# Kernel tuning notes

Hardware: AMD Instinct MI355X
Metric: run time of the kernel (lower is better)

## Reference

```python
import jax, jax.numpy as jnp
import numpy as np
from jax import lax

B, T, H, W = 4, 8, 14, 14
DIM, NH = 768, 8
HD = DIM // NH            # 96, head dim (= depthwise conv channels)
G = 1                     # global_embed_num
N = T * H * W + 1 + G     # 1570 tokens: [global, cls, spatial]
HID = 4 * DIM
BIG = 1.0e8


def ln(x, g, b, eps=1e-5):
    m = jnp.mean(x, axis=-1, keepdims=True)
    v = jnp.mean(jnp.square(x - m), axis=-1, keepdims=True)
    return (x - m) * jax.lax.rsqrt(v + eps) * g + b


def setup_inputs() -> dict:
    key = jax.random.key(0)
    ks = jax.random.split(key, 12)
    s = 0.02
    inp = {
        "x": jax.random.normal(ks[0], (B, N, DIM), jnp.float32),
        "t": T, "h": H, "w": W,
        "norm1_g": jnp.ones((DIM,), jnp.float32),
        "norm1_b": jnp.zeros((DIM,), jnp.float32),
        "qkv_w": jax.random.normal(ks[1], (3 * DIM, DIM), jnp.float32) * s,
        "qkv_b": jnp.zeros((3 * DIM,), jnp.float32),
        "conv_q": jax.random.normal(ks[2], (HD, 1, 3, 3, 3), jnp.float32) * 0.05,
        "nq_g": jnp.ones((HD,), jnp.float32), "nq_b": jnp.zeros((HD,), jnp.float32),
        "conv_k": jax.random.normal(ks[3], (HD, 1, 3, 3, 3), jnp.float32) * 0.05,
        "nk_g": jnp.ones((HD,), jnp.float32), "nk_b": jnp.zeros((HD,), jnp.float32),
        "conv_v": jax.random.normal(ks[4], (HD, 1, 3, 3, 3), jnp.float32) * 0.05,
        "nv_g": jnp.ones((HD,), jnp.float32), "nv_b": jnp.zeros((HD,), jnp.float32),
        "proj_w": jax.random.normal(ks[5], (DIM, DIM), jnp.float32) * s,
        "proj_b": jnp.zeros((DIM,), jnp.float32),
        "norm2_g": jnp.ones((DIM,), jnp.float32),
        "norm2_b": jnp.zeros((DIM,), jnp.float32),
        "fc1_w": jax.random.normal(ks[6], (HID, DIM), jnp.float32) * s,
        "fc1_b": jnp.zeros((HID,), jnp.float32),
        "fc2_w": jax.random.normal(ks[7], (DIM, HID), jnp.float32) * s,
        "fc2_b": jnp.zeros((DIM,), jnp.float32),
    }
    return inp


def _pool(tok, cw, g, b):
    # tok: [B, NH, N, HD] -> depthwise conv3d per head on spatial tokens, then LN
    glob, cls, body = tok[:, :, :G], tok[:, :, G:G + 1], tok[:, :, G + 1:]
    z = body.reshape(B * NH, T, H, W, HD).transpose(0, 4, 1, 2, 3)  # [BN, C, T, H, W]
    z = lax.conv_general_dilated(z, cw, window_strides=(1, 1, 1),
                                 padding=[(1, 1)] * 3, feature_group_count=HD,
                                 dimension_numbers=("NCDHW", "OIDHW", "NCDHW"))
    z = z.reshape(B, NH, HD, T * H * W).transpose(0, 1, 3, 2)       # [B, NH, L, HD]
    z = jnp.concatenate([glob, cls, z], axis=2)                     # splice cls then global
    return ln(z, g, b)


def reference(x, t, h, w, norm1_g, norm1_b, qkv_w, qkv_b,
              conv_q, nq_g, nq_b, conv_k, nk_g, nk_b, conv_v, nv_g, nv_b,
              proj_w, proj_b, norm2_g, norm2_b, fc1_w, fc1_b, fc2_w, fc2_b):
    scale = HD ** (-0.5)
    xn = ln(x, norm1_g, norm1_b)
    qkv = (xn @ qkv_w.T + qkv_b).reshape(B, N, 3, NH, HD)
    qkv = qkv.transpose(2, 0, 3, 1, 4)            # [3, B, NH, N, HD]
    q = _pool(qkv[0], conv_q, nq_g, nq_b)
    k = _pool(qkv[1], conv_k, nk_g, nk_b)
    v = _pool(qkv[2], conv_v, nv_g, nv_b)

    attn = jnp.einsum("bhnd,bhmd->bhnm", q, k) * scale
    # additive offset: BIG everywhere except diagonal and the global columns (rows >= G)
    eye = jnp.eye(N, dtype=attn.dtype)
    off2 = eye * BIG
    off2 = off2.at[G:, :G].set(BIG)
    offset = BIG - off2                            # [N, N]
    attn = jax.nn.softmax(attn - offset, axis=-1)

    o = jnp.einsum("bhnm,bhmd->bhnd", attn, v)     # [B, NH, N, HD]
    o = o.transpose(0, 2, 1, 3).reshape(B, N, DIM)
    o = o @ proj_w.T + proj_b

    x = x + o                                      # pool_skip is None -> identity skip
    x2 = ln(x, norm2_g, norm2_b)
    mlp = jax.nn.gelu(x2 @ fc1_w.T + fc1_b, approximate=False) @ fc2_w.T + fc2_b
    return x + mlp
```

## Files before the change

### kernel.cpp

```cpp
#include <hip/hip_runtime.h>
#include <hip/hip_bf16.h>
#include <cmath>

using bf16 = __hip_bfloat16;
using bf16x8_t = __attribute__((ext_vector_type(8))) short;
using f32x4_t  = __attribute__((ext_vector_type(4))) float;

constexpr int kT = 8;
constexpr int kDIM = 768, kNH = 8, kHD = 96;
constexpr int kN = 1570;
constexpr int kB = 4;
constexpr int kM = kB * kN;
constexpr int kBNH = kB * kNH;
constexpr long kPoolRows  = (long)kBNH * kN;
constexpr long kPoolElems = kPoolRows * kHD;

struct SegTab { const void* src[22]; long start[23]; };

__global__ void detect_kernel(const unsigned* __restrict__ probe,
                              unsigned* __restrict__ flag) {
  *flag = (probe[0] == 0x3F803F80u) ? 1u : 0u;
}

__global__ void convert_kernel(SegTab tab, bf16* __restrict__ cin,
                               const unsigned* __restrict__ flag, long chunks) {
  const bool isb = (*flag != 0u);
  const long stride = (long)gridDim.x * blockDim.x;
  for (long c = (long)blockIdx.x * blockDim.x + threadIdx.x; c < chunks; c += stride) {
    const long e8 = c * 8;
    int lo = 0, hi = 22;
    while (hi - lo > 1) { int mid = (lo + hi) >> 1; if (e8 >= tab.start[mid]) lo = mid; else hi = mid; }
    const long e = e8 - tab.start[lo];
    if (isb) {
      *(bf16x8_t*)(cin + e8) = *(const bf16x8_t*)((const unsigned short*)tab.src[lo] + e);
    } else {
      const float* s = (const float*)tab.src[lo] + e;
      float4 a = *(const float4*)s;
      float4 b = *(const float4*)(s + 4);
      bf16 r[8];
      r[0] = (bf16)a.x; r[1] = (bf16)a.y; r[2] = (bf16)a.z; r[3] = (bf16)a.w;
      r[4] = (bf16)b.x; r[5] = (bf16)b.y; r[6] = (bf16)b.z; r[7] = (bf16)b.w;
      *(bf16x8_t*)(cin + e8) = *(bf16x8_t*)r;
    }
  }
}

__device__ __forceinline__ void gload_lds16(const bf16* g, bf16* l) {
  __builtin_amdgcn_global_load_lds(
      (const __attribute__((address_space(1))) unsigned int*)g,
      (__attribute__((address_space(3))) unsigned int*)l, 16, 0, 0);
}

template<int EPI, int DUAL>
__launch_bounds__(512, 1)
__global__ void gemm_bt(const bf16* __restrict__ A, const bf16* __restrict__ Wt,
                        const bf16* __restrict__ bias, const bf16* __restrict__ res,
                        bf16* __restrict__ C, float* __restrict__ Cf,
                        const unsigned* __restrict__ flagp,
                        int M, int K, int Nout, int tiles_n)
{
  __shared__ bf16 shm[73728];
  const int tid  = threadIdx.x;
  const int lane = tid & 63;
  const int wv   = tid >> 6;
  const int wr   = wv & 3, wc = wv >> 2;

  const int nwg = gridDim.x;
  const int tiles_m = nwg / tiles_n;
  const int q8 = nwg >> 3, r8 = nwg & 7;
  const int xcd = blockIdx.x & 7, slot = blockIdx.x >> 3;
  const int base = (xcd < r8) ? xcd * (q8 + 1) : r8 * (q8 + 1) + (xcd - r8) * q8;
  const int lin = base + slot;
  const int paired = (tiles_m & ~1) * tiles_n;
  int tmi, tni;
  if (lin < paired) {
    const int grp = lin / (2 * tiles_n);
    const int rem = lin - grp * 2 * tiles_n;
    tmi = grp * 2 + (rem & 1);
    tni = rem >> 1;
  } else {
    tmi = tiles_m - 1;
    tni = lin - paired;
  }
  const long tile_m = (long)tmi * 256;
  const long tile_n = (long)tni * 128;

  bool isb = true;
  if constexpr (DUAL) isb = (*flagp != 0u);

  f32x4_t zero = {0.f, 0.f, 0.f, 0.f};
  f32x4_t acc[4][4];
#pragma unroll
  for (int i = 0; i < 4; ++i)
#pragma unroll
    for (int j = 0; j < 4; ++j) acc[i][j] = zero;

  const int rb = tid >> 3;
  const int g8 = (((tid & 7) ^ (rb & 7))) * 8;
  const bf16* sA[4];
  const bf16* sB[2];
#pragma unroll
  for (int i = 0; i < 4; ++i) {
    long ar = tile_m + rb + i * 64; if (ar > M - 1) ar = M - 1;
    sA[i] = A + ar * K + g8;
  }
#pragma unroll
  for (int i = 0; i < 2; ++i)
    sB[i] = Wt + (tile_n + rb + i * 64) * K + g8;

  auto stage = [&](int kt, int buf) {
    const long koff = (long)kt << 6;
#pragma unroll
    for (int i = 0; i < 4; ++i)
      gload_lds16(sA[i] + koff, shm + buf * 16384 + i * 4096 + tid * 8);
#pragma unroll
    for (int i = 0; i < 2; ++i)
      gload_lds16(sB[i] + koff, shm + 49152 + buf * 8192 + i * 4096 + tid * 8);
  };

  const int j0 = (((lane >> 4) ^ (lane & 7))) * 8;
  const int j1 = ((((lane >> 4) ^ 4)) ^ (lane & 7)) * 8;
  const int rA0 = wr * 64 + (lane & 15);
  const int rB0 = wc * 64 + (lane & 15);

  const int ksteps = K >> 6;
  stage(0, 0);
  stage(1, 1);
  stage(2, 2);
  asm volatile("s_waitcnt vmcnt(12)" ::: "memory");
  __builtin_amdgcn_s_barrier();

#define KSTEP(BUF, DOPF, PFKT, WAITOP)                                         \
  {                                                                            \
    const bf16* ab = shm + (BUF) * 16384;                                      \
    const bf16* bp = shm + 49152 + (BUF) * 8192;                               \
    bf16x8_t a[4][2], bfr[4][2];                                               \
    _Pragma("unroll")                                                          \
    for (int m = 0; m < 4; ++m) {                                              \
      a[m][0]   = *(const bf16x8_t*)&ab[((rA0 + m * 16) << 6) + j0];           \
      a[m][1]   = *(const bf16x8_t*)&ab[((rA0 + m * 16) << 6) + j1];           \
      bfr[m][0] = *(const bf16x8_t*)&bp[((rB0 + m * 16) << 6) + j0];           \
      bfr[m][1] = *(const bf16x8_t*)&bp[((rB0 + m * 16) << 6) + j1];           \
    }                                                                          \
    asm volatile("s_waitcnt lgkmcnt(0)" ::: "memory");                         \
    __builtin_amdgcn_sched_barrier(0);                                         \
    __builtin_amdgcn_s_barrier();                                              \
    if (DOPF) stage((PFKT), (BUF));                                            \
    __builtin_amdgcn_s_setprio(1);                                             \
    _Pragma("unroll")                                                          \
    for (int m = 0; m < 4; ++m)                                                \
      _Pragma("unroll")                                                        \
      for (int n = 0; n < 4; ++n) {                                            \
        acc[m][n] = __builtin_amdgcn_mfma_f32_16x16x32_bf16(a[m][0], bfr[n][0], acc[m][n], 0, 0, 0); \
        acc[m][n] = __builtin_amdgcn_mfma_f32_16x16x32_bf16(a[m][1], bfr[n][1], acc[m][n], 0, 0, 0); \
      }                                                                        \
    __builtin_amdgcn_s_setprio(0);                                             \
    asm volatile(WAITOP ::: "memory");                                         \
    __builtin_amdgcn_s_barrier();                                              \
  }

  int p = 0;
  for (; p + 5 < ksteps; p += 3) {
    KSTEP(0, true, p + 3, "s_waitcnt vmcnt(12)")
    KSTEP(1, true, p + 4, "s_waitcnt vmcnt(12)")
    KSTEP(2, true, p + 5, "s_waitcnt vmcnt(12)")
  }
  KSTEP(0, false, 0, "s_waitcnt vmcnt(6)")
  KSTEP(1, false, 0, "s_waitcnt vmcnt(0)")
  KSTEP(2, false, 0, "s_waitcnt vmcnt(0)")
#undef KSTEP

  {
    const int cB = wc * 64 + (lane & 15);
    const int rB = wr * 64 + ((lane >> 4) << 2);
#pragma unroll
    for (int n = 0; n < 4; ++n) {
      const int col = cB + n * 16;
      const float bv = (float)bias[tile_n + col];
#pragma unroll
      for (int m = 0; m < 4; ++m)
#pragma unroll
        for (int r = 0; r < 4; ++r)
          shm[(rB + m * 16 + r) * 136 + col] = (bf16)(acc[m][n][r] + bv);
    }
  }
  __syncthreads();
#pragma unroll
  for (int it = 0; it < 8; ++it) {
    const int chunk = tid + it * 512;
    const int row = chunk >> 4;
    const int colc = (chunk & 15) * 8;
    const long grow = tile_m + row;
    if (grow < M) {
      const bf16x8_t v8 = *(const bf16x8_t*)&shm[row * 136 + colc];
      const long gcol = tile_n + colc;
      float f[8];
#pragma unroll
      for (int j = 0; j < 8; ++j) {
        unsigned short u = (unsigned short)v8[j];
        f[j] = __uint_as_float((unsigned)u << 16);
      }
      if constexpr (EPI == 1) {
#pragma unroll
        for (int j = 0; j < 8; ++j) {
          const float v2 = f[j];
          const float zarg = 1.59576912160573f * v2 * (1.f + 0.044715f * v2 * v2);
          f[j] = v2 * __builtin_amdgcn_rcpf(1.f + __expf(-zarg));
        }
      } else if constexpr (EPI == 2) {
        const bf16x8_t rv = *(const bf16x8_t*)&res[grow * Nout + gcol];
#pragma unroll
        for (int j = 0; j < 8; ++j) {
          unsigned short u = (unsigned short)rv[j];
          f[j] += __uint_as_float((unsigned)u << 16);
        }
      }
      if (DUAL && !isb) {
        float4 s0 = {f[0], f[1], f[2], f[3]};
        float4 s1 = {f[4], f[5], f[6], f[7]};
        *(float4*)&Cf[grow * Nout + gcol] = s0;
        *(float4*)&Cf[grow * Nout + gcol + 4] = s1;
      } else {
        bf16 o8[8];
#pragma unroll
        for (int j = 0; j < 8; ++j) o8[j] = (bf16)f[j];
        *(bf16x8_t*)&C[grow * Nout + gcol] = *(bf16x8_t*)o8;
      }
    }
  }
}

__global__ void ln768_kernel(const bf16* __restrict__ x, const bf16* __restrict__ g,
                             const bf16* __restrict__ bta, bf16* __restrict__ y)
{
  const long row = blockIdx.x;
  const int tid = threadIdx.x;
  const bf16* xr = x + row * kDIM;
  float v[3];
  float s = 0.f, ss = 0.f;
#pragma unroll
  for (int i = 0; i < 3; ++i) {
    v[i] = (float)xr[tid + i * 256];
    s += v[i]; ss += v[i] * v[i];
  }
#pragma unroll
  for (int off = 32; off; off >>= 1) {
    s  += __shfl_xor(s, off);
    ss += __shfl_xor(ss, off);
  }
  __shared__ float red[8];
  const int wv = tid >> 6;
  if ((tid & 63) == 0) { red[wv] = s; red[4 + wv] = ss; }
  __syncthreads();
  s  = red[0] + red[1] + red[2] + red[3];
  ss = red[4] + red[5] + red[6] + red[7];
  const float mean = s * (1.f / kDIM);
  const float var  = ss * (1.f / kDIM) - mean * mean;
  const float rstd = rsqrtf(var + 1e-5f);
  bf16* yr = y + row * kDIM;
#pragma unroll
  for (int i = 0; i < 3; ++i) {
    const int c = tid + i * 256;
    yr[c] = (bf16)((v[i] - mean) * rstd * (float)g[c] + (float)bta[c]);
  }
}

__launch_bounds__(256, 4)
__global__ void convpool3_kernel(const bf16* __restrict__ qkv,
                                 const bf16* __restrict__ cwq,
                                 const bf16* __restrict__ cwk,
                                 const bf16* __restrict__ cwv,
                                 bf16* __restrict__ pool)
{
  __shared__ bf16 tile[3 * 256 * 16];
  const int t    = blockIdx.x;
  const int bh   = blockIdx.y;
  const int z    = blockIdx.z;
  const int s    = z / 6, cgrp = z - s * 6;
  const int tid  = threadIdx.x;
  const int b    = bh >> 3, h = bh & 7;

  const bf16* src0 = qkv + (long)(b * kN) * 2304 + s * kDIM + h * kHD + cgrp * 16;

  {
    f32x4_t z4 = {0.f, 0.f, 0.f, 0.f};
    for (int i = tid; i < 3072; i += 256)
      *(f32x4_t*)((char*)tile + (long)i * 16) = z4;
  }
  __syncthreads();

  for (int c = tid; c < 1176; c += 256) {
    const int slice = c / 392;
    const int rem   = c - slice * 392;
    const int p     = rem >> 1;
    const int seg   = rem & 1;
    const int tt    = t + slice - 1;
    if ((unsigned)tt < 8u) {
      const int y = p / 14, x = p - y * 14;
      const int n = 2 + tt * 196 + p;
      const bf16x8_t v = *(const bf16x8_t*)(src0 + (long)n * 2304 + seg * 8);
      *(bf16x8_t*)&tile[slice * 4096 + ((y + 1) * 16 + (x + 1)) * 16 + seg * 8] = v;
    }
  }

  const int dpair = tid & 7;
  const int pg    = tid >> 3;
  const int d0    = cgrp * 16 + dpair * 2;
  const bf16* cw  = (s == 0) ? cwq : (s == 1) ? cwk : cwv;
  float w0[27], w1[27];
#pragma unroll
  for (int i = 0; i < 27; ++i) {
    w0[i] = (float)cw[d0 * 27 + i];
    w1[i] = (float)cw[(d0 + 1) * 27 + i];
  }
  __syncthreads();

  bf16* out0 = pool + (long)s * kPoolElems + (long)bh * kN * kHD;
  for (int p = pg; p < 196; p += 32) {
    const int y = p / 14, x = p - y * 14;
    const char* bp = (const char*)tile + ((y * 16 + x) * 16 + dpair * 2) * 2;
    float a0 = 0.f, a1 = 0.f;
#pragma unroll
    for (int dt = 0; dt < 3; ++dt)
#pragma unroll
      for (int dy = 0; dy < 3; ++dy)
#pragma unroll
        for (int dx = 0; dx < 3; ++dx) {
          const unsigned u = *(const unsigned*)(bp + dt * 8192 + dy * 512 + dx * 32);
          const int i = (dt * 3 + dy) * 3 + dx;
          a0 = fmaf(__uint_as_float(u << 16), w0[i], a0);
          a1 = fmaf(__uint_as_float(u & 0xffff0000u), w1[i], a1);
        }
    const int n = 2 + t * 196 + p;
    bf16 r0 = (bf16)a0, r1 = (bf16)a1;
    unsigned pk = ((unsigned)*(unsigned short*)&r1 << 16) | *(unsigned short*)&r0;
    *(unsigned*)((char*)(out0 + (long)n * kHD + d0)) = pk;
  }
  if (t == 0 && tid < 32) {
    const int tok = tid >> 4, dd = tid & 15;
    out0[(long)tok * kHD + cgrp * 16 + dd] = src0[(long)tok * 2304 + dd];
  }
}

__global__ void ln96_kernel(bf16* __restrict__ pool,
                            const bf16* __restrict__ gq, const bf16* __restrict__ bq,
                            const bf16* __restrict__ gk, const bf16* __restrict__ bk,
                            const bf16* __restrict__ gv, const bf16* __restrict__ bv)
{
  const int z = blockIdx.y;
  bf16* buf = pool + (long)z * kPoolElems;
  const bf16* g  = (z == 0) ? gq : (z == 1) ? gk : gv;
  const bf16* be = (z == 0) ? bq : (z == 1) ? bk : bv;
  const long row = (long)blockIdx.x * 4 + (threadIdx.x >> 6);
  if (row >= kPoolRows) return;
  const int lane = threadIdx.x & 63;
  bf16* p = buf + row * kHD;
  float a0 = 0.f, a1 = 0.f;
  if (lane < 48) {
    a0 = (float)p[lane * 2];
    a1 = (float)p[lane * 2 + 1];
  }
  float sSum = a0 + a1, sSq = a0 * a0 + a1 * a1;
#pragma unroll
  for (int off = 32; off; off >>= 1) {
    sSum += __shfl_xor(sSum, off);
    sSq  += __shfl_xor(sSq, off);
  }
  const float mean = sSum * (1.f / 96);
  const float var  = sSq * (1.f / 96) - mean * mean;
  const float rstd = rsqrtf(var + 1e-5f);
  if (lane < 48) {
    p[lane * 2]     = (bf16)((a0 - mean) * rstd * (float)g[lane * 2]     + (float)be[lane * 2]);
    p[lane * 2 + 1] = (bf16)((a1 - mean) * rstd * (float)g[lane * 2 + 1] + (float)be[lane * 2 + 1]);
  }
}

__global__ void attn_kernel(const bf16* __restrict__ pool, bf16* __restrict__ o)
{
  const long idx = (long)blockIdx.x * 4 + (threadIdx.x >> 6);
  if (idx >= kPoolRows) return;
  const int bh = (int)(idx / kN);
  const int i  = (int)(idx - (long)bh * kN);
  const int lane = threadIdx.x & 63;
  const bf16* qrow  = pool + ((long)bh * kN + i) * kHD;
  const bf16* kbase = pool + kPoolElems + (long)bh * kN * kHD;
  const bf16* vbase = pool + 2 * kPoolElems + (long)bh * kN * kHD;
  float q0 = 0, q1 = 0, ki0 = 0, ki1 = 0, k00 = 0, k01 = 0;
  float vi0 = 0, vi1 = 0, v00 = 0, v01 = 0;
  if (lane < 48) {
    const int c = lane * 2;
    q0  = (float)qrow[c];                  q1  = (float)qrow[c + 1];
    ki0 = (float)kbase[(long)i * kHD + c]; ki1 = (float)kbase[(long)i * kHD + c + 1];
    k00 = (float)kbase[c];                 k01 = (float)kbase[c + 1];
    vi0 = (float)vbase[(long)i * kHD + c]; vi1 = (float)vbase[(long)i * kHD + c + 1];
    v00 = (float)vbase[c];                 v01 = (float)vbase[c + 1];
  }
  float ds = q0 * ki0 + q1 * ki1;
  float dg = q0 * k00 + q1 * k01;
#pragma unroll
  for (int off = 32; off; off >>= 1) {
    ds += __shfl_xor(ds, off);
    dg += __shfl_xor(dg, off);
  }
  float o0, o1;
  if (i == 0) { o0 = v00; o1 = v01; }
  else {
    const float scale = 0.10206207261596575f;
    const float l0 = dg * scale, li = ds * scale;
    const float mx = fmaxf(l0, li);
    const float e0 = __expf(l0 - mx), ei = __expf(li - mx);
    const float inv = 1.f / (e0 + ei);
    o0 = (e0 * v00 + ei * vi0) * inv;
    o1 = (e0 * v01 + ei * vi1) * inv;
  }
  if (lane < 48) {
    const int b = bh >> 3, h = bh & 7;
    bf16* orow = o + ((long)b * kN + i) * kDIM + h * kHD + lane * 2;
    orow[0] = (bf16)o0;
    orow[1] = (bf16)o1;
  }
}

extern "C" void kernel_launch(void* const* d_in, const int* in_sizes, int n_in,
                              void* d_out, int out_size, void* d_ws, size_t ws_size,
                              hipStream_t stream)
{
  const int map[22] = {0,4,5,6,7,8,9,10,11,12,13,14,15,16,17,18,19,20,21,22,23,24};

  char* ws = (char*)d_ws;
  unsigned* flag = (unsigned*)ws;

  size_t off = 256;
  auto take = [&](size_t bytes) {
    size_t r = off;
    off += (bytes + 255) & ~(size_t)255;
    return r;
  };

  SegTab tab;
  long total = 0;
  tab.start[0] = 0;
  for (int j = 0; j < 22; ++j) {
    tab.src[j] = d_in[map[j]];
    total += in_sizes[map[j]];
    tab.start[j + 1] = total;
  }

  bf16* cin = (bf16*)(ws + take((size_t)total * 2));

  bf16* cp[22];
  { long acc = 0;
    for (int j = 0; j < 22; ++j) { cp[j] = cin + acc; acc += in_sizes[map[j]]; } }
  bf16* x_c    = cp[0];
  bf16* n1g_c  = cp[1],  *n1b_c = cp[2];
  bf16* qkvw_c = cp[3],  *qkvb_c = cp[4];
  bf16* cwq_c  = cp[5],  *nqg_c = cp[6],  *nqb_c = cp[7];
  bf16* cwk_c  = cp[8],  *nkg_c = cp[9],  *nkb_c = cp[10];
  bf16* cwv_c  = cp[11], *nvg_c = cp[12], *nvb_c = cp[13];
  bf16* projw_c = cp[14], *projb_c = cp[15];
  bf16* n2g_c  = cp[16], *n2b_c = cp[17];
  bf16* fc1w_c = cp[18], *fc1b_c = cp[19];
  bf16* fc2w_c = cp[20], *fc2b_c = cp[21];

  bf16* qkv  = (bf16*)(ws + take(38584320));
  bf16* xn   = (bf16*)(ws + take(9646080));
  bf16* pool = (bf16*)(ws + take(28938240));
  bf16* x1   = (bf16*)(ws + take(9646080));
  bf16* o   = xn;
  bf16* h1  = qkv;
  bf16* x2n = pool;

  bf16*  out_b = (bf16*)d_out;
  float* out_f = (float*)d_out;

  detect_kernel<<<1, 1, 0, stream>>>((const unsigned*)d_in[4], flag);
  convert_kernel<<<2048, 256, 0, stream>>>(tab, cin, flag, total / 8);

  ln768_kernel<<<kM, 256, 0, stream>>>(x_c, n1g_c, n1b_c, xn);
  gemm_bt<0,0><<<25 * 18, 512, 0, stream>>>(xn, qkvw_c, qkvb_c, nullptr, qkv, nullptr, nullptr, kM, 768, 2304, 18);
  convpool3_kernel<<<dim3(kT, kBNH, 18), 256, 0, stream>>>(qkv, cwq_c, cwk_c, cwv_c, pool);
  ln96_kernel<<<dim3((int)((kPoolRows + 3) / 4), 3), 256, 0, stream>>>(pool, nqg_c, nqb_c, nkg_c, nkb_c, nvg_c, nvb_c);
  attn_kernel<<<(int)((kPoolRows + 3) / 4), 256, 0, stream>>>(pool, o);
  gemm_bt<2,0><<<25 * 6, 512, 0, stream>>>(o, projw_c, projb_c, x_c, x1, nullptr, nullptr, kM, 768, 768, 6);
  ln768_kernel<<<kM, 256, 0, stream>>>(x1, n2g_c, n2b_c, x2n);
  gemm_bt<1,0><<<25 * 24, 512, 0, stream>>>(x2n, fc1w_c, fc1b_c, nullptr, h1, nullptr, nullptr, kM, 768, 3072, 24);
  gemm_bt<2,1><<<25 * 6, 512, 0, stream>>>(h1, fc2w_c, fc2b_c, x1, out_b, out_f, flag, kM, 3072, 768, 6);
}
```

Baseline: 275.0 us.

## Shrink GEMM tiles to 128x128 with BK=32 and 256-thread blocks for occupancy

Reworks the bf16 GEMM from 256x128 tiles with 512 threads and a 64-wide K step to 128x128 tiles with 256 threads and a 32-wide K step. This cuts LDS per block so three blocks can share a CU, and doubles the grid size. The prefetch moves to the start of each step into a rotating third buffer, replacing the old wait-barrier-prefetch sequence and priority hints. The aim is more parallelism and better latency hiding on M=6280. In exchange it loses per-tile data reuse, issues more barriers per unit of K, and has only a two-stage lookahead.

```diff
diff --git a/kernel.cpp b/kernel.cpp
--- a/kernel.cpp
+++ b/kernel.cpp
@@ -52,18 +52,18 @@
 }
 
 template<int EPI, int DUAL>
-__launch_bounds__(512, 1)
+__launch_bounds__(256, 3)
 __global__ void gemm_bt(const bf16* __restrict__ A, const bf16* __restrict__ Wt,
                         const bf16* __restrict__ bias, const bf16* __restrict__ res,
                         bf16* __restrict__ C, float* __restrict__ Cf,
                         const unsigned* __restrict__ flagp,
                         int M, int K, int Nout, int tiles_n)
 {
-  __shared__ bf16 shm[73728];
+  __shared__ bf16 shm[24576];
   const int tid  = threadIdx.x;
   const int lane = tid & 63;
   const int wv   = tid >> 6;
-  const int wr   = wv & 3, wc = wv >> 2;
+  const int wr   = wv >> 1, wc = wv & 1;
 
   const int nwg = gridDim.x;
   const int tiles_m = nwg / tiles_n;
@@ -82,7 +82,7 @@
     tmi = tiles_m - 1;
     tni = lin - paired;
   }
-  const long tile_m = (long)tmi * 256;
+  const long tile_m = (long)tmi * 128;
   const long tile_n = (long)tni * 128;
 
   bool isb = true;
@@ -95,77 +95,65 @@
 #pragma unroll
     for (int j = 0; j < 4; ++j) acc[i][j] = zero;
 
-  const int rb = tid >> 3;
-  const int g8 = (((tid & 7) ^ (rb & 7))) * 8;
-  const bf16* sA[4];
+  const int rb = tid >> 2;
+  const int g8 = (((tid & 3) ^ ((rb >> 1) & 3))) * 8;
+  const bf16* sA[2];
   const bf16* sB[2];
 #pragma unroll
-  for (int i = 0; i < 4; ++i) {
+  for (int i = 0; i < 2; ++i) {
     long ar = tile_m + rb + i * 64; if (ar > M - 1) ar = M - 1;
     sA[i] = A + ar * K + g8;
-  }
-#pragma unroll
-  for (int i = 0; i < 2; ++i)
     sB[i] = Wt + (tile_n + rb + i * 64) * K + g8;
+  }
 
   auto stage = [&](int kt, int buf) {
-    const long koff = (long)kt << 6;
-#pragma unroll
-    for (int i = 0; i < 4; ++i)
-      gload_lds16(sA[i] + koff, shm + buf * 16384 + i * 4096 + tid * 8);
+    const long koff = (long)kt << 5;
 #pragma unroll
     for (int i = 0; i < 2; ++i)
-      gload_lds16(sB[i] + koff, shm + 49152 + buf * 8192 + i * 4096 + tid * 8);
+      gload_lds16(sA[i] + koff, shm + buf * 4096 + i * 2048 + tid * 8);
+#pragma unroll
+    for (int i = 0; i < 2; ++i)
+      gload_lds16(sB[i] + koff, shm + 12288 + buf * 4096 + i * 2048 + tid * 8);
   };
 
-  const int j0 = (((lane >> 4) ^ (lane & 7))) * 8;
-  const int j1 = ((((lane >> 4) ^ 4)) ^ (lane & 7)) * 8;
+  const int j0 = (((lane >> 4) ^ ((lane >> 1) & 3))) * 8;
   const int rA0 = wr * 64 + (lane & 15);
   const int rB0 = wc * 64 + (lane & 15);
 
-  const int ksteps = K >> 6;
+  const int ksteps = K >> 5;
   stage(0, 0);
   stage(1, 1);
-  stage(2, 2);
-  asm volatile("s_waitcnt vmcnt(12)" ::: "memory");
+  asm volatile("s_waitcnt vmcnt(4)" ::: "memory");
   __builtin_amdgcn_s_barrier();
 
 #define KSTEP(BUF, DOPF, PFKT, WAITOP)                                         \
   {                                                                            \
-    const bf16* ab = shm + (BUF) * 16384;                                      \
-    const bf16* bp = shm + 49152 + (BUF) * 8192;                               \
-    bf16x8_t a[4][2], bfr[4][2];                                               \
+    if (DOPF) stage((PFKT), ((BUF) + 2) % 3);                                  \
+    const bf16* ab = shm + (BUF) * 4096;                                       \
+    const bf16* bp = shm + 12288 + (BUF) * 4096;                               \
+    bf16x8_t a[4], bfr[4];                                                     \
     _Pragma("unroll")                                                          \
     for (int m = 0; m < 4; ++m) {                                              \
-      a[m][0]   = *(const bf16x8_t*)&ab[((rA0 + m * 16) << 6) + j0];           \
-      a[m][1]   = *(const bf16x8_t*)&ab[((rA0 + m * 16) << 6) + j1];           \
-      bfr[m][0] = *(const bf16x8_t*)&bp[((rB0 + m * 16) << 6) + j0];           \
-      bfr[m][1] = *(const bf16x8_t*)&bp[((rB0 + m * 16) << 6) + j1];           \
+      a[m]   = *(const bf16x8_t*)&ab[((rA0 + m * 16) << 5) + j0];              \
+      bfr[m] = *(const bf16x8_t*)&bp[((rB0 + m * 16) << 5) + j0];              \
     }                                                                          \
-    asm volatile("s_waitcnt lgkmcnt(0)" ::: "memory");                         \
-    __builtin_amdgcn_sched_barrier(0);                                         \
-    __builtin_amdgcn_s_barrier();                                              \
-    if (DOPF) stage((PFKT), (BUF));                                            \
-    __builtin_amdgcn_s_setprio(1);                                             \
     _Pragma("unroll")                                                          \
     for (int m = 0; m < 4; ++m)                                                \
       _Pragma("unroll")                                                        \
-      for (int n = 0; n < 4; ++n) {                                            \
-        acc[m][n] = __builtin_amdgcn_mfma_f32_16x16x32_bf16(a[m][0], bfr[n][0], acc[m][n], 0, 0, 0); \
-        acc[m][n] = __builtin_amdgcn_mfma_f32_16x16x32_bf16(a[m][1], bfr[n][1], acc[m][n], 0, 0, 0); \
-      }                                                                        \
-    __builtin_amdgcn_s_setprio(0);                                             \
+      for (int n = 0; n < 4; ++n)                                              \
+        acc[m][n] = __builtin_amdgcn_mfma_f32_16x16x32_bf16(a[m], bfr[n], acc[m][n], 0, 0, 0); \
+    asm volatile("s_waitcnt lgkmcnt(0)" ::: "memory");                         \
     asm volatile(WAITOP ::: "memory");                                         \
     __builtin_amdgcn_s_barrier();                                              \
   }
 
   int p = 0;
   for (; p + 5 < ksteps; p += 3) {
-    KSTEP(0, true, p + 3, "s_waitcnt vmcnt(12)")
-    KSTEP(1, true, p + 4, "s_waitcnt vmcnt(12)")
-    KSTEP(2, true, p + 5, "s_waitcnt vmcnt(12)")
-  }
-  KSTEP(0, false, 0, "s_waitcnt vmcnt(6)")
+    KSTEP(0, true, p + 2, "s_waitcnt vmcnt(4)")
+    KSTEP(1, true, p + 3, "s_waitcnt vmcnt(4)")
+    KSTEP(2, true, p + 4, "s_waitcnt vmcnt(4)")
+  }
+  KSTEP(0, true, ksteps - 1, "s_waitcnt vmcnt(4)")
   KSTEP(1, false, 0, "s_waitcnt vmcnt(0)")
   KSTEP(2, false, 0, "s_waitcnt vmcnt(0)")
 #undef KSTEP
@@ -187,7 +175,7 @@
   __syncthreads();
 #pragma unroll
   for (int it = 0; it < 8; ++it) {
-    const int chunk = tid + it * 512;
+    const int chunk = tid + it * 256;
     const int row = chunk >> 4;
     const int colc = (chunk & 15) * 8;
     const long grow = tile_m + row;
@@ -477,12 +465,12 @@
   convert_kernel<<<2048, 256, 0, stream>>>(tab, cin, flag, total / 8);
 
   ln768_kernel<<<kM, 256, 0, stream>>>(x_c, n1g_c, n1b_c, xn);
-  gemm_bt<0,0><<<25 * 18, 512, 0, stream>>>(xn, qkvw_c, qkvb_c, nullptr, qkv, nullptr, nullptr, kM, 768, 2304, 18);
+  gemm_bt<0,0><<<50 * 18, 256, 0, stream>>>(xn, qkvw_c, qkvb_c, nullptr, qkv, nullptr, nullptr, kM, 768, 2304, 18);
   convpool3_kernel<<<dim3(kT, kBNH, 18), 256, 0, stream>>>(qkv, cwq_c, cwk_c, cwv_c, pool);
   ln96_kernel<<<dim3((int)((kPoolRows + 3) / 4), 3), 256, 0, stream>>>(pool, nqg_c, nqb_c, nkg_c, nkb_c, nvg_c, nvb_c);
   attn_kernel<<<(int)((kPoolRows + 3) / 4), 256, 0, stream>>>(pool, o);
-  gemm_bt<2,0><<<25 * 6, 512, 0, stream>>>(o, projw_c, projb_c, x_c, x1, nullptr, nullptr, kM, 768, 768, 6);
+  gemm_bt<2,0><<<50 * 6, 256, 0, stream>>>(o, projw_c, projb_c, x_c, x1, nullptr, nullptr, kM, 768, 768, 6);
   ln768_kernel<<<kM, 256, 0, stream>>>(x1, n2g_c, n2b_c, x2n);
-  gemm_bt<1,0><<<25 * 24, 512, 0, stream>>>(x2n, fc1w_c, fc1b_c, nullptr, h1, nullptr, nullptr, kM, 768, 3072, 24);
-  gemm_bt<2,1><<<25 * 6, 512, 0, stream>>>(h1, fc2w_c, fc2b_c, x1, out_b, out_f, flag, kM, 3072, 768, 6);
-}
+  gemm_bt<1,0><<<50 * 24, 256, 0, stream>>>(x2n, fc1w_c, fc1b_c, nullptr, h1, nullptr, nullptr, kM, 768, 3072, 24);
+  gemm_bt<2,1><<<50 * 6, 256, 0, stream>>>(h1, fc2w_c, fc2b_c, x1, out_b, out_f, flag, kM, 3072, 768, 6);
+}
```

New measurement: 262.2 us. -4.7%, faster.

## Add 256x256-tile GEMM for QKV and FC1, restructure prefetch pipeline

Applied to the files above, without the earlier changes.

Adds a new gemm256 kernel with 256x256 output tiles, BK=32 and a 3-buffer LDS ring, allowing 2 workgroups per CU, and uses it for the QKV and FC1 projections. The larger tiles cut A/B reloads per output element and halve the grid. The existing gemm_bt is also changed to issue the prefetch at the start of each k-step into the buffer two ahead, dropping the mid-step barrier and setprio. The risks are more register pressure from 128 accumulators per thread, and fewer tiles, which could underfill the CUs.

```diff
diff --git a/kernel.cpp b/kernel.cpp
--- a/kernel.cpp
+++ b/kernel.cpp
@@ -51,19 +51,18 @@
       (__attribute__((address_space(3))) unsigned int*)l, 16, 0, 0);
 }
 
-template<int EPI, int DUAL>
-__launch_bounds__(512, 1)
-__global__ void gemm_bt(const bf16* __restrict__ A, const bf16* __restrict__ Wt,
-                        const bf16* __restrict__ bias, const bf16* __restrict__ res,
-                        bf16* __restrict__ C, float* __restrict__ Cf,
-                        const unsigned* __restrict__ flagp,
+template<int EPI>
+__launch_bounds__(512, 2)
+__global__ void gemm256(const bf16* __restrict__ A, const bf16* __restrict__ Wt,
+                        const bf16* __restrict__ bias,
+                        bf16* __restrict__ C,
                         int M, int K, int Nout, int tiles_n)
 {
-  __shared__ bf16 shm[73728];
+  __shared__ bf16 shm[49152];
   const int tid  = threadIdx.x;
   const int lane = tid & 63;
   const int wv   = tid >> 6;
-  const int wr   = wv & 3, wc = wv >> 2;
+  const int wr   = wv >> 2, wc = wv & 3;
 
   const int nwg = gridDim.x;
   const int tiles_m = nwg / tiles_n;
@@ -83,6 +82,162 @@
     tni = lin - paired;
   }
   const long tile_m = (long)tmi * 256;
+  const long tile_n = (long)tni * 256;
+
+  f32x4_t zero = {0.f, 0.f, 0.f, 0.f};
+  f32x4_t acc[8][4];
+#pragma unroll
+  for (int i = 0; i < 8; ++i)
+#pragma unroll
+    for (int j = 0; j < 4; ++j) acc[i][j] = zero;
+
+  const int rb = tid >> 2;
+  const int g8 = (((tid & 3) ^ ((rb >> 1) & 3))) * 8;
+  const bf16* sA[2];
+  const bf16* sB[2];
+#pragma unroll
+  for (int i = 0; i < 2; ++i) {
+    long ar = tile_m + rb + i * 128; if (ar > M - 1) ar = M - 1;
+    sA[i] = A + ar * K + g8;
+    sB[i] = Wt + (tile_n + rb + i * 128) * K + g8;
+  }
+
+  auto stage = [&](int kt, int buf) {
+    const long koff = (long)kt << 5;
+#pragma unroll
+    for (int i = 0; i < 2; ++i)
+      gload_lds16(sA[i] + koff, shm + buf * 8192 + i * 4096 + tid * 8);
+#pragma unroll
+    for (int i = 0; i < 2; ++i)
+      gload_lds16(sB[i] + koff, shm + 24576 + buf * 8192 + i * 4096 + tid * 8);
+  };
+
+  const int j0 = (((lane >> 4) ^ ((lane >> 1) & 3))) * 8;
+  const int rA0 = wr * 128 + (lane & 15);
+  const int rB0 = wc * 64 + (lane & 15);
+
+  const int ksteps = K >> 5;
+  stage(0, 0);
+  stage(1, 1);
+  asm volatile("s_waitcnt vmcnt(4)" ::: "memory");
+  __builtin_amdgcn_s_barrier();
+
+#define KSTEP(BUF, DOPF, PFKT, WAITOP)                                         \
+  {                                                                            \
+    if (DOPF) stage((PFKT), ((BUF) + 2) % 3);                                  \
+    const bf16* ab = shm + (BUF) * 8192;                                       \
+    const bf16* bp = shm + 24576 + (BUF) * 8192;                               \
+    bf16x8_t a[8], bfr[4];                                                     \
+    _Pragma("unroll")                                                          \
+    for (int m = 0; m < 8; ++m)                                                \
+      a[m] = *(const bf16x8_t*)&ab[((rA0 + m * 16) << 5) + j0];                \
+    _Pragma("unroll")                                                          \
+    for (int n = 0; n < 4; ++n)                                                \
+      bfr[n] = *(const bf16x8_t*)&bp[((rB0 + n * 16) << 5) + j0];              \
+    _Pragma("unroll")                                                          \
+    for (int m = 0; m < 8; ++m)                                                \
+      _Pragma("unroll")                                                        \
+      for (int n = 0; n < 4; ++n)                                              \
+        acc[m][n] = __builtin_amdgcn_mfma_f32_16x16x32_bf16(a[m], bfr[n], acc[m][n], 0, 0, 0); \
+    asm volatile("s_waitcnt lgkmcnt(0)" ::: "memory");                         \
+    asm volatile(WAITOP ::: "memory");                                         \
+    __builtin_amdgcn_s_barrier();                                              \
+  }
+
+  int p = 0;
+  for (; p + 5 < ksteps; p += 3) {
+    KSTEP(0, true, p + 2, "s_waitcnt vmcnt(4)")
+    KSTEP(1, true, p + 3, "s_waitcnt vmcnt(4)")
+    KSTEP(2, true, p + 4, "s_waitcnt vmcnt(4)")
+  }
+  KSTEP(0, true, ksteps - 1, "s_waitcnt vmcnt(4)")
+  KSTEP(1, false, 0, "s_waitcnt vmcnt(0)")
+  KSTEP(2, false, 0, "s_waitcnt vmcnt(0)")
+#undef KSTEP
+
+  __syncthreads();
+#pragma unroll
+  for (int pass = 0; pass < 2; ++pass) {
+    if ((wc >> 1) == pass) {
+      const int colL = wc * 64 + (lane & 15) - pass * 128;
+      const int rowW = wr * 128 + ((lane >> 4) << 2);
+#pragma unroll
+      for (int n = 0; n < 4; ++n) {
+        const int col = colL + n * 16;
+        const float bv = (float)bias[tile_n + pass * 128 + col];
+#pragma unroll
+        for (int m = 0; m < 8; ++m)
+#pragma unroll
+          for (int r = 0; r < 4; ++r)
+            shm[(rowW + m * 16 + r) * 136 + col] = (bf16)(acc[m][n][r] + bv);
+      }
+    }
+    __syncthreads();
+#pragma unroll
+    for (int it = 0; it < 8; ++it) {
+      const int chunk = tid + it * 512;
+      const int row = chunk >> 4;
+      const int colc = (chunk & 15) * 8;
+      const long grow = tile_m + row;
+      if (grow < M) {
+        const bf16x8_t v8 = *(const bf16x8_t*)&shm[row * 136 + colc];
+        const long gcol = tile_n + pass * 128 + colc;
+        float f[8];
+#pragma unroll
+        for (int j = 0; j < 8; ++j) {
+          unsigned short u = (unsigned short)v8[j];
+          f[j] = __uint_as_float((unsigned)u << 16);
+        }
+        if constexpr (EPI == 1) {
+#pragma unroll
+          for (int j = 0; j < 8; ++j) {
+            const float v2 = f[j];
+            const float zarg = 1.59576912160573f * v2 * (1.f + 0.044715f * v2 * v2);
+            f[j] = v2 * __builtin_amdgcn_rcpf(1.f + __expf(-zarg));
+          }
+        }
+        bf16 o8[8];
+#pragma unroll
+        for (int j = 0; j < 8; ++j) o8[j] = (bf16)f[j];
+        *(bf16x8_t*)&C[grow * Nout + gcol] = *(bf16x8_t*)o8;
+      }
+    }
+    __syncthreads();
+  }
+}
+
+template<int EPI, int DUAL>
+__launch_bounds__(512, 1)
+__global__ void gemm_bt(const bf16* __restrict__ A, const bf16* __restrict__ Wt,
+                        const bf16* __restrict__ bias, const bf16* __restrict__ res,
+                        bf16* __restrict__ C, float* __restrict__ Cf,
+                        const unsigned* __restrict__ flagp,
+                        int M, int K, int Nout, int tiles_n)
+{
+  __shared__ bf16 shm[73728];
+  const int tid  = threadIdx.x;
+  const int lane = tid & 63;
+  const int wv   = tid >> 6;
+  const int wr   = wv & 3, wc = wv >> 2;
+
+  const int nwg = gridDim.x;
+  const int tiles_m = nwg / tiles_n;
+  const int q8 = nwg >> 3, r8 = nwg & 7;
+  const int xcd = blockIdx.x & 7, slot = blockIdx.x >> 3;
+  const int base = (xcd < r8) ? xcd * (q8 + 1) : r8 * (q8 + 1) + (xcd - r8) * q8;
+  const int lin = base + slot;
+  const int paired = (tiles_m & ~1) * tiles_n;
+  int tmi, tni;
+  if (lin < paired) {
+    const int grp = lin / (2 * tiles_n);
+    const int rem = lin - grp * 2 * tiles_n;
+    tmi = grp * 2 + (rem & 1);
+    tni = rem >> 1;
+  } else {
+    tmi = tiles_m - 1;
+    tni = lin - paired;
+  }
+  const long tile_m = (long)tmi * 256;
   const long tile_n = (long)tni * 128;
 
   bool isb = true;
@@ -126,12 +281,12 @@
   const int ksteps = K >> 6;
   stage(0, 0);
   stage(1, 1);
-  stage(2, 2);
-  asm volatile("s_waitcnt vmcnt(12)" ::: "memory");
+  asm volatile("s_waitcnt vmcnt(6)" ::: "memory");
   __builtin_amdgcn_s_barrier();
 
 #define KSTEP(BUF, DOPF, PFKT, WAITOP)                                         \
   {                                                                            \
+    if (DOPF) stage((PFKT), ((BUF) + 2) % 3);                                  \
     const bf16* ab = shm + (BUF) * 16384;                                      \
     const bf16* bp = shm + 49152 + (BUF) * 8192;                               \
     bf16x8_t a[4][2], bfr[4][2];                                               \
@@ -142,11 +297,6 @@
       bfr[m][0] = *(const bf16x8_t*)&bp[((rB0 + m * 16) << 6) + j0];           \
       bfr[m][1] = *(const bf16x8_t*)&bp[((rB0 + m * 16) << 6) + j1];           \
     }                                                                          \
-    asm volatile("s_waitcnt lgkmcnt(0)" ::: "memory");                         \
-    __builtin_amdgcn_sched_barrier(0);                                         \
-    __builtin_amdgcn_s_barrier();                                              \
-    if (DOPF) stage((PFKT), (BUF));                                            \
-    __builtin_amdgcn_s_setprio(1);                                             \
     _Pragma("unroll")                                                          \
     for (int m = 0; m < 4; ++m)                                                \
       _Pragma("unroll")                                                        \
@@ -154,18 +304,18 @@
         acc[m][n] = __builtin_amdgcn_mfma_f32_16x16x32_bf16(a[m][0], bfr[n][0], acc[m][n], 0, 0, 0); \
         acc[m][n] = __builtin_amdgcn_mfma_f32_16x16x32_bf16(a[m][1], bfr[n][1], acc[m][n], 0, 0, 0); \
       }                                                                        \
-    __builtin_amdgcn_s_setprio(0);                                             \
+    asm volatile("s_waitcnt lgkmcnt(0)" ::: "memory");                         \
     asm volatile(WAITOP ::: "memory");                                         \
     __builtin_amdgcn_s_barrier();                                              \
   }
 
   int p = 0;
   for (; p + 5 < ksteps; p += 3) {
-    KSTEP(0, true, p + 3, "s_waitcnt vmcnt(12)")
-    KSTEP(1, true, p + 4, "s_waitcnt vmcnt(12)")
-    KSTEP(2, true, p + 5, "s_waitcnt vmcnt(12)")
-  }
-  KSTEP(0, false, 0, "s_waitcnt vmcnt(6)")
+    KSTEP(0, true, p + 2, "s_waitcnt vmcnt(6)")
+    KSTEP(1, true, p + 3, "s_waitcnt vmcnt(6)")
+    KSTEP(2, true, p + 4, "s_waitcnt vmcnt(6)")
+  }
+  KSTEP(0, true, ksteps - 1, "s_waitcnt vmcnt(6)")
   KSTEP(1, false, 0, "s_waitcnt vmcnt(0)")
   KSTEP(2, false, 0, "s_waitcnt vmcnt(0)")
 #undef KSTEP
@@ -477,12 +627,12 @@
   convert_kernel<<<2048, 256, 0, stream>>>(tab, cin, flag, total / 8);
 
   ln768_kernel<<<kM, 256, 0, stream>>>(x_c, n1g_c, n1b_c, xn);
-  gemm_bt<0,0><<<25 * 18, 512, 0, stream>>>(xn, qkvw_c, qkvb_c, nullptr, qkv, nullptr, nullptr, kM, 768, 2304, 18);
+  gemm256<0><<<25 * 9, 512, 0, stream>>>(xn, qkvw_c, qkvb_c, qkv, kM, 768, 2304, 9);
   convpool3_kernel<<<dim3(kT, kBNH, 18), 256, 0, stream>>>(qkv, cwq_c, cwk_c, cwv_c, pool);
   ln96_kernel<<<dim3((int)((kPoolRows + 3) / 4), 3), 256, 0, stream>>>(pool, nqg_c, nqb_c, nkg_c, nkb_c, nvg_c, nvb_c);
   attn_kernel<<<(int)((kPoolRows + 3) / 4), 256, 0, stream>>>(pool, o);
   gemm_bt<2,0><<<25 * 6, 512, 0, stream>>>(o, projw_c, projb_c, x_c, x1, nullptr, nullptr, kM, 768, 768, 6);
   ln768_kernel<<<kM, 256, 0, stream>>>(x1, n2g_c, n2b_c, x2n);
-  gemm_bt<1,0><<<25 * 24, 512, 0, stream>>>(x2n, fc1w_c, fc1b_c, nullptr, h1, nullptr, nullptr, kM, 768, 3072, 24);
+  gemm256<1><<<25 * 12, 512, 0, stream>>>(x2n, fc1w_c, fc1b_c, h1, kM, 768, 3072, 12);
   gemm_bt<2,1><<<25 * 6, 512, 0, stream>>>(h1, fc2w_c, fc2b_c, x1, out_b, out_f, flag, kM, 3072, 768, 6);
 }
```

Result: faster. 260.2 us (median of 3 runs) (-5.4%).
